# Performance work log

Measured on AMD Instinct MI355X. Metric: run time of the kernel, lower is better.

The kernel has to match this reference:

```python
import jax, jax.numpy as jnp
import numpy as np

PARTITIONS = 8
TWO_PI = 2.0 * np.pi
B, N, T, D_RES = 4096, 128, 20, 64


def setup_inputs() -> dict:
    key = jax.random.key(0)
    k1, k2, k3, k4 = jax.random.split(key, 4)
    return {
        "ego_traj_2d": jax.random.normal(k1, (B, T, 2), dtype=jnp.float32),
        "nei_traj_2d": jax.random.normal(k2, (B, N, T, 2), dtype=jnp.float32),
        "f_resonance": jax.random.normal(k3, (B, N, D_RES), dtype=jnp.float32),
        "W_ce": jax.random.normal(k4, (2, D_RES), dtype=jnp.float32) * 0.1,
        "b_ce": jnp.zeros((D_RES,), dtype=jnp.float32),
    }


def reference(ego_traj_2d, nei_traj_2d, f_resonance, W_ce, b_ce):
    # relative position of each neighbor at the last frame: [B, N, 2]
    nei_rel_pos = nei_traj_2d[..., -1, :] - ego_traj_2d[..., -1, :][..., None, :]

    f_distance = jnp.linalg.norm(nei_rel_pos, axis=-1)                # [B, N]
    f_direction = jnp.arctan2(nei_rel_pos[..., 0], nei_rel_pos[..., 1])
    f_direction = jnp.mod(f_direction, TWO_PI)                        # [B, N]

    angle_indices = (f_direction / (TWO_PI / PARTITIONS)).astype(jnp.int32)

    # neighbor validity mask: all-zero padded trajectories are invalid
    nei_mask = (jnp.sum(nei_traj_2d, axis=(-1, -2)) != 0).astype(jnp.int32)  # [B, N]
    angle_indices = angle_indices * nei_mask - (1 - nei_mask)  # invalid -> -1

    # one-hot bin membership replaces the per-partition python loop: [B, N, P]
    onehot = (angle_indices[..., None] == jnp.arange(PARTITIONS, dtype=jnp.int32)).astype(jnp.float32)
    n = jnp.sum(onehot, axis=-2) + 1e-4                               # [B, P]

    sum_dist = jnp.einsum("bn,bnp->bp", f_distance, onehot)
    sum_dir = jnp.einsum("bn,bnp->bp", f_direction, onehot)
    resonance_circle = jnp.einsum("bnd,bnp->bpd", f_resonance, onehot) / n[..., None]  # [B, P, D_RES]

    scan_circle = jnp.stack([sum_dist / n, sum_dir / n], axis=-1)     # [B, P, 2]

    # TrajEncoding(2, d//2, ReLU): single dense layer with ReLU
    f_scan = jax.nn.relu(scan_circle @ W_ce + b_ce)                   # [B, P, D_RES]

    return jnp.concatenate([resonance_circle, f_scan], axis=-1)      # [B, P, 2*D_RES]
```

## Files before the change

### kernel.cpp

```cpp
#include <hip/hip_runtime.h>
#include <math.h>

namespace {
constexpr int kB = 4096, kN = 128, kT = 20, kD = 64, kP = 8;
constexpr float kTwoPi = 6.28318530717958647692f;
constexpr float kBinW  = 0.78539816339744830962f;
}

__global__ __launch_bounds__(256)
void circle_kernel(const float* __restrict__ ego,
                   const float* __restrict__ nei,
                   const float* __restrict__ fres,
                   const float* __restrict__ Wce,
                   const float* __restrict__ bce,
                   float* __restrict__ out) {
  const int b   = blockIdx.x;
  const int tid = threadIdx.x;
  const int lane = tid & 63;
  const int wv   = tid >> 6;

  __shared__ float  s_nsum[kN];
  __shared__ float  s_lastx[kN], s_lasty[kN];
  __shared__ int    s_bin[kN];
  __shared__ float  s_cnt[kP], s_sdist[kP], s_sdir[kP];
  __shared__ float4 s_res[4][kP][kD / 4];

  if (tid < kN) s_nsum[tid] = 0.0f;
  if (tid < kP) { s_cnt[tid] = 0.0f; s_sdist[tid] = 0.0f; s_sdir[tid] = 0.0f; }
  __syncthreads();

  const float4* nb4 = reinterpret_cast<const float4*>(nei + (size_t)b * (kN * kT * 2));
  #pragma unroll
  for (int i = 0; i < 5; ++i) {
    const int j = tid + 256 * i;
    const float4 v = nb4[j];
    const int n = j / 10;
    atomicAdd(&s_nsum[n], (v.x + v.y) + (v.z + v.w));
    if (j - n * 10 == 9) { s_lastx[n] = v.z; s_lasty[n] = v.w; }
  }
  const float egx = ego[(size_t)b * (kT * 2) + (kT - 1) * 2 + 0];
  const float egy = ego[(size_t)b * (kT * 2) + (kT - 1) * 2 + 1];
  __syncthreads();

  if (tid < kN) {
    const float rx = s_lastx[tid] - egx;
    const float ry = s_lasty[tid] - egy;
    const float dist = sqrtf(rx * rx + ry * ry);
    float dir = (float)atan2((double)rx, (double)ry);
    if (dir < 0.0f) dir += kTwoPi;
    int idx = (int)(dir / kBinW);
    if (s_nsum[tid] == 0.0f) idx = -1;
    s_bin[tid] = idx;
    if (idx >= 0 && idx < kP) {
      atomicAdd(&s_cnt[idx],  1.0f);
      atomicAdd(&s_sdist[idx], dist);
      atomicAdd(&s_sdir[idx],  dir);
    }
  }
  __syncthreads();

  const float4* r4 = reinterpret_cast<const float4*>(fres + (size_t)b * (kN * kD));
  const int rsub = lane >> 4;
  const int dq   = lane & 15;
  float acc[kP][4];
  #pragma unroll
  for (int p = 0; p < kP; ++p) { acc[p][0] = acc[p][1] = acc[p][2] = acc[p][3] = 0.0f; }
  #pragma unroll
  for (int k = 0; k < 8; ++k) {
    const int n = wv * 32 + k * 4 + rsub;
    const float4 v = r4[n * 16 + dq];
    const int bin = s_bin[n];
    #pragma unroll
    for (int p = 0; p < kP; ++p) {
      const float mf = (bin == p) ? 1.0f : 0.0f;
      acc[p][0] = fmaf(v.x, mf, acc[p][0]);
      acc[p][1] = fmaf(v.y, mf, acc[p][1]);
      acc[p][2] = fmaf(v.z, mf, acc[p][2]);
      acc[p][3] = fmaf(v.w, mf, acc[p][3]);
    }
  }
  #pragma unroll
  for (int p = 0; p < kP; ++p) {
    #pragma unroll
    for (int j = 0; j < 4; ++j) {
      float x = acc[p][j];
      x += __shfl_xor(x, 16, 64);
      x += __shfl_xor(x, 32, 64);
      acc[p][j] = x;
    }
  }
  if (lane < 16) {
    #pragma unroll
    for (int p = 0; p < kP; ++p)
      s_res[wv][p][dq] = make_float4(acc[p][0], acc[p][1], acc[p][2], acc[p][3]);
  }
  __syncthreads();

  const int p = tid >> 5;
  const int q = tid & 31;
  const float nf = s_cnt[p] + 1e-4f;
  float* ob = out + (size_t)b * (kP * 2 * kD) + p * (2 * kD);
  if (q < 16) {
    const float4 a = s_res[0][p][q], c = s_res[1][p][q];
    const float4 d2 = s_res[2][p][q], e = s_res[3][p][q];
    float4 o;
    o.x = (a.x + c.x + d2.x + e.x) / nf;
    o.y = (a.y + c.y + d2.y + e.y) / nf;
    o.z = (a.z + c.z + d2.z + e.z) / nf;
    o.w = (a.w + c.w + d2.w + e.w) / nf;
    reinterpret_cast<float4*>(ob)[q] = o;
  } else {
    const int d = (q - 16) * 4;
    const float s0 = s_sdist[p] / nf;
    const float s1 = s_sdir[p] / nf;
    float4 o;
    o.x = fmaxf(s0 * Wce[d + 0] + s1 * Wce[kD + d + 0] + bce[d + 0], 0.0f);
    o.y = fmaxf(s0 * Wce[d + 1] + s1 * Wce[kD + d + 1] + bce[d + 1], 0.0f);
    o.z = fmaxf(s0 * Wce[d + 2] + s1 * Wce[kD + d + 2] + bce[d + 2], 0.0f);
    o.w = fmaxf(s0 * Wce[d + 3] + s1 * Wce[kD + d + 3] + bce[d + 3], 0.0f);
    reinterpret_cast<float4*>(ob + kD)[q - 16] = o;
  }
}

extern "C" void kernel_launch(void* const* d_in, const int* in_sizes, int n_in,
                              void* d_out, int out_size, void* d_ws, size_t ws_size,
                              hipStream_t stream) {
  const float* ego  = (const float*)d_in[0];
  const float* nei  = (const float*)d_in[1];
  const float* fres = (const float*)d_in[2];
  const float* Wce  = (const float*)d_in[3];
  const float* bce  = (const float*)d_in[4];
  float* out = (float*)d_out;
  hipLaunchKernelGGL(circle_kernel, dim3(kB), dim3(256), 0, stream,
                     ego, nei, fres, Wce, bce, out);
}
```

Baseline: 263.3 us.

## Split fused kernel into binning and gather kernels via workspace

Splits the single fused kernel into two launches: a binning kernel that reduces neighbor trajectories with two threads per neighbor and shuffles instead of shared atomics, and a gather kernel that reads bins and bin statistics from a global workspace. The aim is to decouple the trajectory reduction from the resonance accumulation so each kernel has less serialization and shared-memory work. In exchange it adds a second launch, a global round trip for bins and stats, and reliance on the workspace being large enough.

After: 257.8 us. 1.02x faster.

```diff
diff --git a/kernel.cpp b/kernel.cpp
--- a/kernel.cpp
+++ b/kernel.cpp
@@ -8,68 +8,79 @@
 }
 
 __global__ __launch_bounds__(256)
-void circle_kernel(const float* __restrict__ ego,
-                   const float* __restrict__ nei,
-                   const float* __restrict__ fres,
-                   const float* __restrict__ Wce,
-                   const float* __restrict__ bce,
-                   float* __restrict__ out) {
-  const int b   = blockIdx.x;
-  const int tid = threadIdx.x;
-  const int lane = tid & 63;
-  const int wv   = tid >> 6;
-
-  __shared__ float  s_nsum[kN];
-  __shared__ float  s_lastx[kN], s_lasty[kN];
-  __shared__ int    s_bin[kN];
-  __shared__ float  s_cnt[kP], s_sdist[kP], s_sdir[kP];
-  __shared__ float4 s_res[4][kP][kD / 4];
-
-  if (tid < kN) s_nsum[tid] = 0.0f;
-  if (tid < kP) { s_cnt[tid] = 0.0f; s_sdist[tid] = 0.0f; s_sdir[tid] = 0.0f; }
+void bin_kernel(const float* __restrict__ ego,
+                const float* __restrict__ nei,
+                int*   __restrict__ wbin,
+                float* __restrict__ wcnt,
+                float* __restrict__ wdist,
+                float* __restrict__ wdir) {
+  const int b = blockIdx.x, tid = threadIdx.x;
+  const int n = tid >> 1, h = tid & 1;
+  __shared__ float s_cnt[kP], s_d[kP], s_th[kP];
+  if (tid < kP) { s_cnt[tid] = 0.f; s_d[tid] = 0.f; s_th[tid] = 0.f; }
   __syncthreads();
 
-  const float4* nb4 = reinterpret_cast<const float4*>(nei + (size_t)b * (kN * kT * 2));
-  #pragma unroll
-  for (int i = 0; i < 5; ++i) {
-    const int j = tid + 256 * i;
-    const float4 v = nb4[j];
-    const int n = j / 10;
-    atomicAdd(&s_nsum[n], (v.x + v.y) + (v.z + v.w));
-    if (j - n * 10 == 9) { s_lastx[n] = v.z; s_lasty[n] = v.w; }
-  }
-  const float egx = ego[(size_t)b * (kT * 2) + (kT - 1) * 2 + 0];
-  const float egy = ego[(size_t)b * (kT * 2) + (kT - 1) * 2 + 1];
-  __syncthreads();
+  const float4* p4 = reinterpret_cast<const float4*>(
+      nei + (size_t)b * (kN * kT * 2) + n * 40 + h * 20);
+  const float4 v0 = p4[0], v1 = p4[1], v2 = p4[2], v3 = p4[3], v4 = p4[4];
+  float s = ((v0.x + v0.y) + (v0.z + v0.w)) + ((v1.x + v1.y) + (v1.z + v1.w))
+          + ((v2.x + v2.y) + (v2.z + v2.w)) + ((v3.x + v3.y) + (v3.z + v3.w))
+          + ((v4.x + v4.y) + (v4.z + v4.w));
+  const float tot = s + __shfl_xor(s, 1, 64);
+  const float lx = __shfl_xor(v4.z, 1, 64);
+  const float ly = __shfl_xor(v4.w, 1, 64);
 
-  if (tid < kN) {
-    const float rx = s_lastx[tid] - egx;
-    const float ry = s_lasty[tid] - egy;
+  if (h == 0) {
+    const float egx = ego[(size_t)b * (kT * 2) + 38];
+    const float egy = ego[(size_t)b * (kT * 2) + 39];
+    const float rx = lx - egx, ry = ly - egy;
     const float dist = sqrtf(rx * rx + ry * ry);
     float dir = (float)atan2((double)rx, (double)ry);
     if (dir < 0.0f) dir += kTwoPi;
     int idx = (int)(dir / kBinW);
-    if (s_nsum[tid] == 0.0f) idx = -1;
-    s_bin[tid] = idx;
+    if (tot == 0.0f) idx = -1;
+    wbin[(size_t)b * kN + n] = idx;
     if (idx >= 0 && idx < kP) {
-      atomicAdd(&s_cnt[idx],  1.0f);
-      atomicAdd(&s_sdist[idx], dist);
-      atomicAdd(&s_sdir[idx],  dir);
+      atomicAdd(&s_cnt[idx], 1.0f);
+      atomicAdd(&s_d[idx],  dist);
+      atomicAdd(&s_th[idx], dir);
     }
   }
   __syncthreads();
+  if (tid < kP) {
+    wcnt [b * kP + tid] = s_cnt[tid];
+    wdist[b * kP + tid] = s_d[tid];
+    wdir [b * kP + tid] = s_th[tid];
+  }
+}
+
+__global__ __launch_bounds__(256)
+void gather_kernel(const float* __restrict__ fres,
+                   const int*   __restrict__ wbin,
+                   const float* __restrict__ wcnt,
+                   const float* __restrict__ wdist,
+                   const float* __restrict__ wdir,
+                   const float* __restrict__ Wce,
+                   const float* __restrict__ bce,
+                   float* __restrict__ out) {
+  const int b = blockIdx.x, tid = threadIdx.x;
+  const int lane = tid & 63, wv = tid >> 6;
+  const int rsub = lane >> 4;
+  const int dq   = lane & 15;
+  __shared__ float4 s_res[4][kP][kD / 4];
 
   const float4* r4 = reinterpret_cast<const float4*>(fres + (size_t)b * (kN * kD));
-  const int rsub = lane >> 4;
-  const int dq   = lane & 15;
+  const int* bb = wbin + (size_t)b * kN;
+
   float acc[kP][4];
   #pragma unroll
-  for (int p = 0; p < kP; ++p) { acc[p][0] = acc[p][1] = acc[p][2] = acc[p][3] = 0.0f; }
+  for (int p = 0; p < kP; ++p) { acc[p][0] = acc[p][1] = acc[p][2] = acc[p][3] = 0.f; }
+
   #pragma unroll
   for (int k = 0; k < 8; ++k) {
     const int n = wv * 32 + k * 4 + rsub;
     const float4 v = r4[n * 16 + dq];
-    const int bin = s_bin[n];
+    const int bin = bb[n];
     #pragma unroll
     for (int p = 0; p < kP; ++p) {
       const float mf = (bin == p) ? 1.0f : 0.0f;
@@ -96,9 +107,8 @@
   }
   __syncthreads();
 
-  const int p = tid >> 5;
-  const int q = tid & 31;
-  const float nf = s_cnt[p] + 1e-4f;
+  const int p = tid >> 5, q = tid & 31;
+  const float nf = wcnt[b * kP + p] + 1e-4f;
   float* ob = out + (size_t)b * (kP * 2 * kD) + p * (2 * kD);
   if (q < 16) {
     const float4 a = s_res[0][p][q], c = s_res[1][p][q];
@@ -111,8 +121,8 @@
     reinterpret_cast<float4*>(ob)[q] = o;
   } else {
     const int d = (q - 16) * 4;
-    const float s0 = s_sdist[p] / nf;
-    const float s1 = s_sdir[p] / nf;
+    const float s0 = wdist[b * kP + p] / nf;
+    const float s1 = wdir [b * kP + p] / nf;
     float4 o;
     o.x = fmaxf(s0 * Wce[d + 0] + s1 * Wce[kD + d + 0] + bce[d + 0], 0.0f);
     o.y = fmaxf(s0 * Wce[d + 1] + s1 * Wce[kD + d + 1] + bce[d + 1], 0.0f);
@@ -131,6 +141,14 @@
   const float* Wce  = (const float*)d_in[3];
   const float* bce  = (const float*)d_in[4];
   float* out = (float*)d_out;
-  hipLaunchKernelGGL(circle_kernel, dim3(kB), dim3(256), 0, stream,
-                     ego, nei, fres, Wce, bce, out);
+
+  int*   wbin  = (int*)d_ws;
+  float* wcnt  = (float*)((char*)d_ws + (size_t)kB * kN * sizeof(int));
+  float* wdist = wcnt  + kB * kP;
+  float* wdir  = wdist + kB * kP;
+
+  hipLaunchKernelGGL(bin_kernel, dim3(kB), dim3(256), 0, stream,
+                     ego, nei, wbin, wcnt, wdist, wdir);
+  hipLaunchKernelGGL(gather_kernel, dim3(kB), dim3(256), 0, stream,
+                     fres, wbin, wcnt, wdist, wdir, Wce, bce, out);
 }
```

## Prefetch resonance features into registers early and replace shared atomics with partial sums

Applied to the files above, without the earlier changes.

Issues the f_resonance float4 loads at kernel start into registers, so they overlap the neighbor-trajectory loads and the angle/binning phase instead of waiting until after two barriers. It also replaces per-element shared-memory atomicAdd for the validity sums with plain stores of partial sums, which one thread per neighbor then adds up. This drops the initial barrier and atomic contention, at the cost of more live registers (32 extra floats) and a larger shared buffer, which may lower occupancy.

Measured after the change: 264.2 us. About the same (+0.3%).

```diff
diff --git a/kernel.cpp b/kernel.cpp
--- a/kernel.cpp
+++ b/kernel.cpp
@@ -8,68 +8,77 @@
 }
 
 __global__ __launch_bounds__(256)
-void circle_kernel(const float* __restrict__ ego,
-                   const float* __restrict__ nei,
-                   const float* __restrict__ fres,
-                   const float* __restrict__ Wce,
-                   const float* __restrict__ bce,
-                   float* __restrict__ out) {
-  const int b   = blockIdx.x;
-  const int tid = threadIdx.x;
-  const int lane = tid & 63;
-  const int wv   = tid >> 6;
+void circle_fused(const float* __restrict__ ego,
+                  const float* __restrict__ nei,
+                  const float* __restrict__ fres,
+                  const float* __restrict__ Wce,
+                  const float* __restrict__ bce,
+                  float* __restrict__ out) {
+  const int b = blockIdx.x, tid = threadIdx.x;
+  const int lane = tid & 63, wv = tid >> 6;
+  const int rsub = lane >> 4;
+  const int dq   = lane & 15;
 
-  __shared__ float  s_nsum[kN];
-  __shared__ float  s_lastx[kN], s_lasty[kN];
+  __shared__ float  s_psum[kN * 10];
+  __shared__ float  s_last[kN * 2];
   __shared__ int    s_bin[kN];
-  __shared__ float  s_cnt[kP], s_sdist[kP], s_sdir[kP];
+  __shared__ float  s_cnt[kP], s_d[kP], s_th[kP];
   __shared__ float4 s_res[4][kP][kD / 4];
 
-  if (tid < kN) s_nsum[tid] = 0.0f;
-  if (tid < kP) { s_cnt[tid] = 0.0f; s_sdist[tid] = 0.0f; s_sdir[tid] = 0.0f; }
-  __syncthreads();
+  if (tid < kP) { s_cnt[tid] = 0.f; s_d[tid] = 0.f; s_th[tid] = 0.f; }
+
+  const float4* r4 = reinterpret_cast<const float4*>(fres + (size_t)b * (kN * kD));
+  float4 rv[8];
+  #pragma unroll
+  for (int k = 0; k < 8; ++k) {
+    const int n = wv * 32 + k * 4 + rsub;
+    rv[k] = r4[n * 16 + dq];
+  }
 
   const float4* nb4 = reinterpret_cast<const float4*>(nei + (size_t)b * (kN * kT * 2));
   #pragma unroll
   for (int i = 0; i < 5; ++i) {
     const int j = tid + 256 * i;
     const float4 v = nb4[j];
+    s_psum[j] = (v.x + v.y) + (v.z + v.w);
     const int n = j / 10;
-    atomicAdd(&s_nsum[n], (v.x + v.y) + (v.z + v.w));
-    if (j - n * 10 == 9) { s_lastx[n] = v.z; s_lasty[n] = v.w; }
+    if (j - n * 10 == 9) { s_last[2 * n] = v.z; s_last[2 * n + 1] = v.w; }
   }
-  const float egx = ego[(size_t)b * (kT * 2) + (kT - 1) * 2 + 0];
-  const float egy = ego[(size_t)b * (kT * 2) + (kT - 1) * 2 + 1];
+  #pragma unroll
+  for (int k = 0; k < 8; ++k)
+    asm volatile("" : "+v"(rv[k].x), "+v"(rv[k].y), "+v"(rv[k].z), "+v"(rv[k].w));
   __syncthreads();
 
   if (tid < kN) {
-    const float rx = s_lastx[tid] - egx;
-    const float ry = s_lasty[tid] - egy;
+    float tot = 0.f;
+    #pragma unroll
+    for (int k = 0; k < 10; ++k) tot += s_psum[tid * 10 + k];
+    const float egx = ego[(size_t)b * (kT * 2) + 38];
+    const float egy = ego[(size_t)b * (kT * 2) + 39];
+    const float rx = s_last[2 * tid] - egx;
+    const float ry = s_last[2 * tid + 1] - egy;
     const float dist = sqrtf(rx * rx + ry * ry);
     float dir = (float)atan2((double)rx, (double)ry);
     if (dir < 0.0f) dir += kTwoPi;
     int idx = (int)(dir / kBinW);
-    if (s_nsum[tid] == 0.0f) idx = -1;
+    if (tot == 0.0f) idx = -1;
     s_bin[tid] = idx;
     if (idx >= 0 && idx < kP) {
-      atomicAdd(&s_cnt[idx],  1.0f);
-      atomicAdd(&s_sdist[idx], dist);
-      atomicAdd(&s_sdir[idx],  dir);
+      atomicAdd(&s_cnt[idx], 1.0f);
+      atomicAdd(&s_d[idx],  dist);
+      atomicAdd(&s_th[idx], dir);
     }
   }
   __syncthreads();
 
-  const float4* r4 = reinterpret_cast<const float4*>(fres + (size_t)b * (kN * kD));
-  const int rsub = lane >> 4;
-  const int dq   = lane & 15;
   float acc[kP][4];
   #pragma unroll
-  for (int p = 0; p < kP; ++p) { acc[p][0] = acc[p][1] = acc[p][2] = acc[p][3] = 0.0f; }
+  for (int p = 0; p < kP; ++p) { acc[p][0] = acc[p][1] = acc[p][2] = acc[p][3] = 0.f; }
   #pragma unroll
   for (int k = 0; k < 8; ++k) {
     const int n = wv * 32 + k * 4 + rsub;
-    const float4 v = r4[n * 16 + dq];
     const int bin = s_bin[n];
+    const float4 v = rv[k];
     #pragma unroll
     for (int p = 0; p < kP; ++p) {
       const float mf = (bin == p) ? 1.0f : 0.0f;
@@ -96,8 +105,7 @@
   }
   __syncthreads();
 
-  const int p = tid >> 5;
-  const int q = tid & 31;
+  const int p = tid >> 5, q = tid & 31;
   const float nf = s_cnt[p] + 1e-4f;
   float* ob = out + (size_t)b * (kP * 2 * kD) + p * (2 * kD);
   if (q < 16) {
@@ -111,8 +119,8 @@
     reinterpret_cast<float4*>(ob)[q] = o;
   } else {
     const int d = (q - 16) * 4;
-    const float s0 = s_sdist[p] / nf;
-    const float s1 = s_sdir[p] / nf;
+    const float s0 = s_d[p] / nf;
+    const float s1 = s_th[p] / nf;
     float4 o;
     o.x = fmaxf(s0 * Wce[d + 0] + s1 * Wce[kD + d + 0] + bce[d + 0], 0.0f);
     o.y = fmaxf(s0 * Wce[d + 1] + s1 * Wce[kD + d + 1] + bce[d + 1], 0.0f);
@@ -131,6 +139,6 @@
   const float* Wce  = (const float*)d_in[3];
   const float* bce  = (const float*)d_in[4];
   float* out = (float*)d_out;
-  hipLaunchKernelGGL(circle_kernel, dim3(kB), dim3(256), 0, stream,
+  hipLaunchKernelGGL(circle_fused, dim3(kB), dim3(256), 0, stream,
                      ego, nei, fres, Wce, bce, out);
 }
```

## Map one batch element per wavefront with shuffle reductions instead of shared memory

Applied to the files above, without the earlier changes.

Each 64-lane wavefront now handles one batch element instead of one block of 256 threads per element. All shared-memory atomics and block barriers are replaced by register accumulation and wave shuffles for the neighbor sums, bin statistics and resonance accumulation. The intent is to remove barrier and LDS atomic overhead and raise occupancy. The trade-off is per-lane strided loads of f_resonance (64 floats per row, coalesced across lanes), scalar rather than float4 output stores, and a long serial loop of 128 neighbors per wave.

Result: slower. 283.5 us (+7.7%).

```diff
diff --git a/kernel.cpp b/kernel.cpp
--- a/kernel.cpp
+++ b/kernel.cpp
@@ -7,118 +7,93 @@
 constexpr float kBinW  = 0.78539816339744830962f;
 }
 
-__global__ __launch_bounds__(256)
-void circle_kernel(const float* __restrict__ ego,
-                   const float* __restrict__ nei,
-                   const float* __restrict__ fres,
-                   const float* __restrict__ Wce,
-                   const float* __restrict__ bce,
-                   float* __restrict__ out) {
-  const int b   = blockIdx.x;
-  const int tid = threadIdx.x;
-  const int lane = tid & 63;
-  const int wv   = tid >> 6;
+__global__ __launch_bounds__(256, 4)
+void circle_wave(const float* __restrict__ ego,
+                 const float* __restrict__ nei,
+                 const float* __restrict__ fres,
+                 const float* __restrict__ Wce,
+                 const float* __restrict__ bce,
+                 float* __restrict__ out) {
+  const int lane = threadIdx.x & 63;
+  const int w    = threadIdx.x >> 6;
+  const int b    = blockIdx.x * 4 + w;
+  const int h    = lane & 1;
+  const int m    = lane >> 1;
 
-  __shared__ float  s_nsum[kN];
-  __shared__ float  s_lastx[kN], s_lasty[kN];
-  __shared__ int    s_bin[kN];
-  __shared__ float  s_cnt[kP], s_sdist[kP], s_sdir[kP];
-  __shared__ float4 s_res[4][kP][kD / 4];
+  const float egx = ego[(size_t)b * 40 + 38];
+  const float egy = ego[(size_t)b * 40 + 39];
 
-  if (tid < kN) s_nsum[tid] = 0.0f;
-  if (tid < kP) { s_cnt[tid] = 0.0f; s_sdist[tid] = 0.0f; s_sdir[tid] = 0.0f; }
-  __syncthreads();
-
-  const float4* nb4 = reinterpret_cast<const float4*>(nei + (size_t)b * (kN * kT * 2));
+  int   binq[4];
+  float distq[4], dirq[4];
+  const float4* nb4 = reinterpret_cast<const float4*>(nei) + (size_t)b * 1280;
   #pragma unroll
-  for (int i = 0; i < 5; ++i) {
-    const int j = tid + 256 * i;
-    const float4 v = nb4[j];
-    const int n = j / 10;
-    atomicAdd(&s_nsum[n], (v.x + v.y) + (v.z + v.w));
-    if (j - n * 10 == 9) { s_lastx[n] = v.z; s_lasty[n] = v.w; }
-  }
-  const float egx = ego[(size_t)b * (kT * 2) + (kT - 1) * 2 + 0];
-  const float egy = ego[(size_t)b * (kT * 2) + (kT - 1) * 2 + 1];
-  __syncthreads();
-
-  if (tid < kN) {
-    const float rx = s_lastx[tid] - egx;
-    const float ry = s_lasty[tid] - egy;
+  for (int q = 0; q < 4; ++q) {
+    const int n = q * 32 + m;
+    const float4* p4 = nb4 + n * 10 + h * 5;
+    const float4 v0 = p4[0], v1 = p4[1], v2 = p4[2], v3 = p4[3], v4 = p4[4];
+    float s = ((v0.x + v0.y) + (v0.z + v0.w)) + ((v1.x + v1.y) + (v1.z + v1.w))
+            + ((v2.x + v2.y) + (v2.z + v2.w)) + ((v3.x + v3.y) + (v3.z + v3.w))
+            + ((v4.x + v4.y) + (v4.z + v4.w));
+    const float tot = s + __shfl_xor(s, 1, 64);
+    const float lx  = __shfl_xor(v4.z, 1, 64);
+    const float ly  = __shfl_xor(v4.w, 1, 64);
+    const float rx = lx - egx, ry = ly - egy;
     const float dist = sqrtf(rx * rx + ry * ry);
     float dir = (float)atan2((double)rx, (double)ry);
     if (dir < 0.0f) dir += kTwoPi;
     int idx = (int)(dir / kBinW);
-    if (s_nsum[tid] == 0.0f) idx = -1;
-    s_bin[tid] = idx;
-    if (idx >= 0 && idx < kP) {
-      atomicAdd(&s_cnt[idx],  1.0f);
-      atomicAdd(&s_sdist[idx], dist);
-      atomicAdd(&s_sdir[idx],  dir);
+    if (h == 1 || tot == 0.0f) idx = -1;
+    binq[q] = idx; distq[q] = dist; dirq[q] = dir;
+  }
+
+  float cnt[kP], sd[kP], sth[kP];
+  #pragma unroll
+  for (int p = 0; p < kP; ++p) {
+    float c = 0.f, d = 0.f, t = 0.f;
+    #pragma unroll
+    for (int q = 0; q < 4; ++q) {
+      const bool hit = (binq[q] == p);
+      c += hit ? 1.0f : 0.0f;
+      d += hit ? distq[q] : 0.0f;
+      t += hit ? dirq[q] : 0.0f;
+    }
+    #pragma unroll
+    for (int o = 1; o < 64; o <<= 1) {
+      c += __shfl_xor(c, o, 64);
+      d += __shfl_xor(d, o, 64);
+      t += __shfl_xor(t, o, 64);
+    }
+    cnt[p] = c; sd[p] = d; sth[p] = t;
+  }
+
+  const float* rb = fres + (size_t)b * (kN * kD) + lane;
+  float acc[kP];
+  #pragma unroll
+  for (int p = 0; p < kP; ++p) acc[p] = 0.f;
+  #pragma unroll
+  for (int q = 0; q < 4; ++q) {
+    const int bq = binq[q];
+    #pragma unroll 16
+    for (int j = 0; j < 32; ++j) {
+      const float v  = rb[(q * 32 + j) * kD];
+      const int   bn = __shfl(bq, 2 * j, 64);
+      #pragma unroll
+      for (int p = 0; p < kP; ++p)
+        acc[p] += (bn == p) ? v : 0.0f;
     }
   }
-  __syncthreads();
 
-  const float4* r4 = reinterpret_cast<const float4*>(fres + (size_t)b * (kN * kD));
-  const int rsub = lane >> 4;
-  const int dq   = lane & 15;
-  float acc[kP][4];
-  #pragma unroll
-  for (int p = 0; p < kP; ++p) { acc[p][0] = acc[p][1] = acc[p][2] = acc[p][3] = 0.0f; }
-  #pragma unroll
-  for (int k = 0; k < 8; ++k) {
-    const int n = wv * 32 + k * 4 + rsub;
-    const float4 v = r4[n * 16 + dq];
-    const int bin = s_bin[n];
-    #pragma unroll
-    for (int p = 0; p < kP; ++p) {
-      const float mf = (bin == p) ? 1.0f : 0.0f;
-      acc[p][0] = fmaf(v.x, mf, acc[p][0]);
-      acc[p][1] = fmaf(v.y, mf, acc[p][1]);
-      acc[p][2] = fmaf(v.z, mf, acc[p][2]);
-      acc[p][3] = fmaf(v.w, mf, acc[p][3]);
-    }
-  }
+  const float w0 = Wce[lane];
+  const float w1 = Wce[kD + lane];
+  const float bc = bce[lane];
+  float* ob = out + (size_t)b * (kP * 2 * kD);
   #pragma unroll
   for (int p = 0; p < kP; ++p) {
-    #pragma unroll
-    for (int j = 0; j < 4; ++j) {
-      float x = acc[p][j];
-      x += __shfl_xor(x, 16, 64);
-      x += __shfl_xor(x, 32, 64);
-      acc[p][j] = x;
-    }
-  }
-  if (lane < 16) {
-    #pragma unroll
-    for (int p = 0; p < kP; ++p)
-      s_res[wv][p][dq] = make_float4(acc[p][0], acc[p][1], acc[p][2], acc[p][3]);
-  }
-  __syncthreads();
-
-  const int p = tid >> 5;
-  const int q = tid & 31;
-  const float nf = s_cnt[p] + 1e-4f;
-  float* ob = out + (size_t)b * (kP * 2 * kD) + p * (2 * kD);
-  if (q < 16) {
-    const float4 a = s_res[0][p][q], c = s_res[1][p][q];
-    const float4 d2 = s_res[2][p][q], e = s_res[3][p][q];
-    float4 o;
-    o.x = (a.x + c.x + d2.x + e.x) / nf;
-    o.y = (a.y + c.y + d2.y + e.y) / nf;
-    o.z = (a.z + c.z + d2.z + e.z) / nf;
-    o.w = (a.w + c.w + d2.w + e.w) / nf;
-    reinterpret_cast<float4*>(ob)[q] = o;
-  } else {
-    const int d = (q - 16) * 4;
-    const float s0 = s_sdist[p] / nf;
-    const float s1 = s_sdir[p] / nf;
-    float4 o;
-    o.x = fmaxf(s0 * Wce[d + 0] + s1 * Wce[kD + d + 0] + bce[d + 0], 0.0f);
-    o.y = fmaxf(s0 * Wce[d + 1] + s1 * Wce[kD + d + 1] + bce[d + 1], 0.0f);
-    o.z = fmaxf(s0 * Wce[d + 2] + s1 * Wce[kD + d + 2] + bce[d + 2], 0.0f);
-    o.w = fmaxf(s0 * Wce[d + 3] + s1 * Wce[kD + d + 3] + bce[d + 3], 0.0f);
-    reinterpret_cast<float4*>(ob + kD)[q - 16] = o;
+    const float nf = cnt[p] + 1e-4f;
+    ob[p * 128 + lane] = acc[p] / nf;
+    const float s0 = sd[p] / nf, s1 = sth[p] / nf;
+    ob[p * 128 + kD + lane] =
+        fmaxf(fmaf(s0, w0, fmaf(s1, w1, bc)), 0.0f);
   }
 }
 
@@ -131,6 +106,6 @@
   const float* Wce  = (const float*)d_in[3];
   const float* bce  = (const float*)d_in[4];
   float* out = (float*)d_out;
-  hipLaunchKernelGGL(circle_kernel, dim3(kB), dim3(256), 0, stream,
+  hipLaunchKernelGGL(circle_wave, dim3(kB / 4), dim3(256), 0, stream,
                      ego, nei, fres, Wce, bce, out);
 }
```
